# Performance work log

Hardware: AMD Instinct MI355X
Metric: run time of the kernel (lower is better)

Reference implementation:

```python
import jax, jax.numpy as jnp
import numpy as np

N_NODES = 50000
N_EDGES = 800000
IN_F = 128
HEADS = 8
D_HEAD = 16  # out_features // num_heads = 128 // 8


def setup_inputs() -> dict:
    key = jax.random.key(0)
    k1, k2, k3, k4, k5 = jax.random.split(key, 5)
    x = jax.random.normal(k1, (N_NODES, IN_F), dtype=jnp.float32)
    edge_index = jax.random.randint(k2, (2, N_EDGES), 0, N_NODES, dtype=jnp.int64)
    # nn.Linear weight is [out, in]; xavier-ish scale
    W = jax.random.normal(k3, (HEADS * D_HEAD, IN_F), dtype=jnp.float32) * (1.0 / np.sqrt(IN_F))
    a_src = jax.random.normal(k4, (HEADS, D_HEAD), dtype=jnp.float32) * (1.0 / np.sqrt(D_HEAD))
    a_dst = jax.random.normal(k5, (HEADS, D_HEAD), dtype=jnp.float32) * (1.0 / np.sqrt(D_HEAD))
    return {"x": x, "edge_index": edge_index, "W": W, "a_src": a_src, "a_dst": a_dst}


def reference(x, edge_index, W, a_src, a_dst):
    N = x.shape[0]
    H, D = a_src.shape
    # h = W x, reshaped to [N, H, D]
    h = (x @ W.T).reshape(N, H, D)
    src, dst = edge_index[0], edge_index[1]
    # per-node attention logits, then gather per-edge (same math as gathering h first)
    s_src = jnp.einsum("nhd,hd->nh", h, a_src)  # [N, H]
    s_dst = jnp.einsum("nhd,hd->nh", h, a_dst)  # [N, H]
    attn = jax.nn.leaky_relu(s_src[src] + s_dst[dst], negative_slope=0.2)  # [E, H]
    # torch scatter_reduce amax onto a zeros tensor -> max is clamped at 0
    attn_max = jnp.maximum(jax.ops.segment_max(attn, dst, num_segments=N), 0.0)  # [N, H]
    e = jnp.exp(attn - attn_max[dst])  # [E, H]
    attn_sum = jax.ops.segment_sum(e, dst, num_segments=N)  # [N, H]
    alpha = e / (attn_sum[dst] + 1e-10)  # [E, H] (dropout is identity in eval)
    msg = h[src] * alpha[..., None]  # [E, H, D]
    out = jax.ops.segment_sum(msg, dst, num_segments=N)  # [N, H, D]
    return out.reshape(N, H * D)
```

## Files before the change

kernel.cpp:

```cpp
#include <hip/hip_runtime.h>
#include <hip/hip_bf16.h>

#define N_NODES 50000
#define N_EDGES 800000
#define HEADS 8
#define MAXDEG 64
#define NPB 4
#define NMFMA ((N_NODES + 127) / 128)
#define NBINB 391
#define NBUCK 128
#define BUCK_NODES 391
#define BUCK_CAP 12288

using frag_ab = __attribute__((ext_vector_type(8))) short;
using frag_cd = __attribute__((ext_vector_type(4))) float;

static __device__ __forceinline__ short f2bs(float v) {
    __hip_bfloat16 b = __float2bfloat16(v);
    return *(short*)&b;
}

__global__ __launch_bounds__(256) void k_wc(const float* __restrict__ W,
                                            const float* __restrict__ a_src,
                                            const float* __restrict__ a_dst,
                                            __hip_bfloat16* __restrict__ Wcb,
                                            int* __restrict__ gcount) {
    int tid = blockIdx.x * 256 + threadIdx.x;
    if (tid < NBUCK) gcount[tid] = 0;
    if (tid >= 144 * 128) return;
    int r = tid >> 7, k = tid & 127;
    float v;
    if (r < 128) {
        v = W[tid];
    } else {
        int hd = (r - 128) & 7;
        const float* av = (r < 136) ? a_src : a_dst;
        v = 0.f;
        #pragma unroll
        for (int d = 0; d < 16; ++d)
            v += av[hd * 16 + d] * W[(size_t)(hd * 16 + d) * 128 + k];
    }
    Wcb[tid] = __float2bfloat16(v);
}

__global__ __launch_bounds__(256) void k_fm(const float* __restrict__ x,
                                            const __hip_bfloat16* __restrict__ Wcb,
                                            __hip_bfloat16* __restrict__ hb,
                                            float* __restrict__ s_src,
                                            float* __restrict__ s_dst,
                                            const int* __restrict__ ei,
                                            int* __restrict__ gcount,
                                            int2* __restrict__ bbuf) {
    __shared__ short Ws[144][136];
    const int t = threadIdx.x;

    if (blockIdx.x >= NMFMA) {
        __shared__ int hist[NBUCK];
        __shared__ int basei[NBUCK];
        const int fb = blockIdx.x - NMFMA;
        for (int i = t; i < NBUCK; i += 256) hist[i] = 0;
        __syncthreads();

        const int e0 = fb * 2048 + t * 8;
        const bool active = (e0 + 8 <= N_EDGES);
        int srcs[8], dsts[8], bks[8];
        if (active) {
            int4 s0 = *(const int4*)(ei + e0);
            int4 s1 = *(const int4*)(ei + e0 + 4);
            int4 d0 = *(const int4*)(ei + N_EDGES + e0);
            int4 d1 = *(const int4*)(ei + N_EDGES + e0 + 4);
            srcs[0] = s0.x; srcs[1] = s0.y; srcs[2] = s0.z; srcs[3] = s0.w;
            srcs[4] = s1.x; srcs[5] = s1.y; srcs[6] = s1.z; srcs[7] = s1.w;
            dsts[0] = d0.x; dsts[1] = d0.y; dsts[2] = d0.z; dsts[3] = d0.w;
            dsts[4] = d1.x; dsts[5] = d1.y; dsts[6] = d1.z; dsts[7] = d1.w;
            #pragma unroll
            for (int u = 0; u < 8; ++u) {
                bks[u] = dsts[u] / BUCK_NODES;
                atomicAdd(&hist[bks[u]], 1);
            }
        }
        __syncthreads();
        if (t < NBUCK) {
            int h = hist[t];
            basei[t] = h ? atomicAdd(&gcount[t], h) : 0;
            hist[t] = 0;
        }
        __syncthreads();
        if (active) {
            #pragma unroll
            for (int u = 0; u < 8; ++u) {
                int off = atomicAdd(&hist[bks[u]], 1);
                int pos = basei[bks[u]] + off;
                if (pos < BUCK_CAP)
                    bbuf[bks[u] * BUCK_CAP + pos] = make_int2(srcs[u], dsts[u]);
            }
        }
        return;
    }

    for (int i = t; i < 144 * 16; i += 256) {
        int r = i >> 4, c = (i & 15) << 3;
        frag_ab v = *(const frag_ab*)((const short*)Wcb + (size_t)r * 128 + c);
        *(frag_ab*)&Ws[r][c] = v;
    }
    __syncthreads();

    const int wave = t >> 6, lane = t & 63;
    const int rb0 = blockIdx.x * 128 + wave * 16;
    if (rb0 >= N_NODES) return;
    const int rb1 = rb0 + 64;
    const int m16 = lane & 15, kg = lane >> 4;
    const int arow0 = min(rb0 + m16, N_NODES - 1);
    const int arow1 = min(rb1 + m16, N_NODES - 1);
    const float* ab0 = x + (size_t)arow0 * 128 + kg * 8;
    const float* ab1 = x + (size_t)arow1 * 128 + kg * 8;

    frag_cd acc[2][9];
    #pragma unroll
    for (int r = 0; r < 2; ++r)
        #pragma unroll
        for (int j = 0; j < 9; ++j) acc[r][j] = (frag_cd){0.f, 0.f, 0.f, 0.f};

    #pragma unroll
    for (int ks = 0; ks < 4; ++ks) {
        float4 p0 = *(const float4*)(ab0 + ks * 32);
        float4 p1 = *(const float4*)(ab0 + ks * 32 + 4);
        float4 q0 = *(const float4*)(ab1 + ks * 32);
        float4 q1 = *(const float4*)(ab1 + ks * 32 + 4);
        frag_ab af0, af1;
        af0[0] = f2bs(p0.x); af0[1] = f2bs(p0.y); af0[2] = f2bs(p0.z); af0[3] = f2bs(p0.w);
        af0[4] = f2bs(p1.x); af0[5] = f2bs(p1.y); af0[6] = f2bs(p1.z); af0[7] = f2bs(p1.w);
        af1[0] = f2bs(q0.x); af1[1] = f2bs(q0.y); af1[2] = f2bs(q0.z); af1[3] = f2bs(q0.w);
        af1[4] = f2bs(q1.x); af1[5] = f2bs(q1.y); af1[6] = f2bs(q1.z); af1[7] = f2bs(q1.w);
        #pragma unroll
        for (int nt = 0; nt < 9; ++nt) {
            frag_ab bf = *(const frag_ab*)&Ws[nt * 16 + m16][ks * 32 + kg * 8];
            acc[0][nt] = __builtin_amdgcn_mfma_f32_16x16x32_bf16(af0, bf, acc[0][nt], 0, 0, 0);
            acc[1][nt] = __builtin_amdgcn_mfma_f32_16x16x32_bf16(af1, bf, acc[1][nt], 0, 0, 0);
        }
    }

    #pragma unroll
    for (int r = 0; r < 2; ++r) {
        int rbase = r ? rb1 : rb0;
        #pragma unroll
        for (int nt = 0; nt < 9; ++nt) {
            #pragma unroll
            for (int j = 0; j < 4; ++j) {
                int row = rbase + kg * 4 + j;
                if (row >= N_NODES) continue;
                int col = nt * 16 + m16;
                float v = acc[r][nt][j];
                if (col < 128)      hb[(size_t)row * 128 + col] = __float2bfloat16(v);
                else if (col < 136) s_src[row * 8 + (col - 128)] = v;
                else                s_dst[row * 8 + (col - 136)] = v;
            }
        }
    }
}

__global__ __launch_bounds__(256) void k_ell(const int2* __restrict__ bbuf,
                                             const int* __restrict__ gcount,
                                             int* __restrict__ cursor,
                                             int* __restrict__ csr_ell) {
    __shared__ int cur[BUCK_NODES];
    const int b = blockIdx.x;
    const int t = threadIdx.x;
    const int lo = b * BUCK_NODES;
    const int hi = min(lo + BUCK_NODES, N_NODES);
    const int ncur = hi - lo;
    for (int i = t; i < ncur; i += 256) cur[i] = 0;
    __syncthreads();
    const int cnt = min(gcount[b], BUCK_CAP);
    for (int i = t; i < cnt; i += 256) {
        int2 e = bbuf[(size_t)b * BUCK_CAP + i];
        int pos = atomicAdd(&cur[e.y - lo], 1);
        if (pos < MAXDEG) csr_ell[e.y * MAXDEG + pos] = e.x;
    }
    __syncthreads();
    for (int i = t; i < ncur; i += 256) cursor[lo + i] = cur[i];
}

__global__ __launch_bounds__(256) void k_gather(const int* __restrict__ csr_ell,
                                                const int* __restrict__ cursor,
                                                const float* __restrict__ s_src,
                                                const float* __restrict__ s_dst,
                                                const __hip_bfloat16* __restrict__ hb,
                                                float* __restrict__ out) {
    __shared__ int   csr_l[NPB][MAXDEG];
    __shared__ float sa[NPB][MAXDEG][9];
    const int slot = threadIdx.x >> 6;
    const int lane = threadIdx.x & 63;
    const int n = blockIdx.x * NPB + slot;
    if (n >= N_NODES) return;
    const int hd8 = lane >> 3, l8 = lane & 7;
    const int deg = min(cursor[n], MAXDEG);
    const float sdst = s_dst[n * 8 + hd8];

    if (lane < deg) csr_l[slot][lane] = csr_ell[n * MAXDEG + lane];

    float m = 0.f;
    for (int j = l8; j < deg; j += 8) {
        float a = s_src[csr_l[slot][j] * 8 + hd8] + sdst;
        a = a > 0.f ? a : 0.2f * a;
        sa[slot][j][hd8] = a;
        m = fmaxf(m, a);
    }
    #pragma unroll
    for (int mask = 1; mask <= 4; mask <<= 1)
        m = fmaxf(m, __shfl_xor(m, mask));

    float s = 0.f;
    for (int j = l8; j < deg; j += 8) {
        float w = __expf(sa[slot][j][hd8] - m);
        sa[slot][j][hd8] = w;
        s += w;
    }
    #pragma unroll
    for (int mask = 1; mask <= 4; mask <<= 1)
        s += __shfl_xor(s, mask);
    float rcp = 1.0f / (s + 1e-10f);

    const int q = lane >> 4;
    const int fl = lane & 15;
    const int hd = fl >> 1;
    const float rcpq = __shfl(rcp, hd * 8);

    const unsigned short* hbs = (const unsigned short*)hb;
    float acc[8] = {0.f, 0.f, 0.f, 0.f, 0.f, 0.f, 0.f, 0.f};

    int j = 0;
    for (; j + 16 <= deg; j += 16) {
        int  jj0 = j + q,      jj1 = j + 4 + q,  jj2 = j + 8 + q,  jj3 = j + 12 + q;
        int  s0 = csr_l[slot][jj0], s1 = csr_l[slot][jj1];
        int  s2 = csr_l[slot][jj2], s3 = csr_l[slot][jj3];
        float w0 = sa[slot][jj0][hd], w1 = sa[slot][jj1][hd];
        float w2 = sa[slot][jj2][hd], w3 = sa[slot][jj3][hd];
        uint4 v0 = *(const uint4*)(hbs + (size_t)s0 * 128 + fl * 8);
        uint4 v1 = *(const uint4*)(hbs + (size_t)s1 * 128 + fl * 8);
        uint4 v2 = *(const uint4*)(hbs + (size_t)s2 * 128 + fl * 8);
        uint4 v3 = *(const uint4*)(hbs + (size_t)s3 * 128 + fl * 8);
        #define ACC8(vv, ww) \
            acc[0] += (ww) * __uint_as_float((vv).x << 16); \
            acc[1] += (ww) * __uint_as_float((vv).x & 0xffff0000u); \
            acc[2] += (ww) * __uint_as_float((vv).y << 16); \
            acc[3] += (ww) * __uint_as_float((vv).y & 0xffff0000u); \
            acc[4] += (ww) * __uint_as_float((vv).z << 16); \
            acc[5] += (ww) * __uint_as_float((vv).z & 0xffff0000u); \
            acc[6] += (ww) * __uint_as_float((vv).w << 16); \
            acc[7] += (ww) * __uint_as_float((vv).w & 0xffff0000u);
        ACC8(v0, w0) ACC8(v1, w1) ACC8(v2, w2) ACC8(v3, w3)
    }
    for (; j + 4 <= deg; j += 4) {
        int jj = j + q;
        int src = csr_l[slot][jj];
        float w = sa[slot][jj][hd];
        uint4 v = *(const uint4*)(hbs + (size_t)src * 128 + fl * 8);
        ACC8(v, w)
    }
    if (j < deg) {
        int jj = j + q;
        if (jj < deg) {
            int src = csr_l[slot][jj];
            float w = sa[slot][jj][hd];
            uint4 v = *(const uint4*)(hbs + (size_t)src * 128 + fl * 8);
            ACC8(v, w)
        }
    }
    #undef ACC8

    #pragma unroll
    for (int k = 0; k < 8; ++k) {
        acc[k] += __shfl_xor(acc[k], 16);
        acc[k] += __shfl_xor(acc[k], 32);
    }
    if (q == 0) {
        float4 o0 = { acc[0] * rcpq, acc[1] * rcpq, acc[2] * rcpq, acc[3] * rcpq };
        float4 o1 = { acc[4] * rcpq, acc[5] * rcpq, acc[6] * rcpq, acc[7] * rcpq };
        *(float4*)(out + (size_t)n * 128 + fl * 8)     = o0;
        *(float4*)(out + (size_t)n * 128 + fl * 8 + 4) = o1;
    }
}

extern "C" void kernel_launch(void* const* d_in, const int* in_sizes, int n_in,
                              void* d_out, int out_size, void* d_ws, size_t ws_size,
                              hipStream_t stream) {
    const float* x     = (const float*)d_in[0];
    const int*   ei    = (const int*)d_in[1];
    const float* W     = (const float*)d_in[2];
    const float* a_src = (const float*)d_in[3];
    const float* a_dst = (const float*)d_in[4];
    float* out = (float*)d_out;

    char* ws = (char*)d_ws;
    __hip_bfloat16* hb      = (__hip_bfloat16*)(ws);
    __hip_bfloat16* Wcb     = (__hip_bfloat16*)(ws + 12800000);
    float*          s_src   = (float*)(ws + 12840000);
    float*          s_dst   = (float*)(ws + 14440000);
    int*            cursor  = (int*)  (ws + 16040000);
    int*            gcount  = (int*)  (ws + 16240000);
    int*            csr_ell = (int*)  (ws + 16241024);
    int2*           bbuf    = (int2*) (ws + 29041024);

    k_wc    <<<(144 * 128 + 255) / 256, 256, 0, stream>>>(W, a_src, a_dst, Wcb, gcount);
    k_fm    <<<NMFMA + NBINB, 256, 0, stream>>>(x, Wcb, hb, s_src, s_dst, ei, gcount, bbuf);
    k_ell   <<<NBUCK, 256, 0, stream>>>(bbuf, gcount, cursor, csr_ell);
    k_gather<<<(N_NODES + NPB - 1) / NPB, 256, 0, stream>>>(csr_ell, cursor, s_src, s_dst, hb, out);
}
```

Baseline: 84.15 us.

## Fold weight prep into GEMM kernel, drop softmax max pass, pad gather loop

Removes the separate weight-combination kernel. Each GEMM block now converts W to bf16 and computes the a_src/a_dst projected rows directly into shared memory, and the bucket counters are cleared with a memset. In the gather kernel, the softmax max-subtraction pass is dropped so exponentials are taken directly on the logits. The edge loop is also padded to multiples of 16 with zero weights, which removes the remainder loops. The trade-offs are redundant per-block weight computation and a risk of exp overflow if logits become large.

```diff
diff --git a/kernel.cpp b/kernel.cpp
--- a/kernel.cpp
+++ b/kernel.cpp
@@ -20,31 +20,10 @@
     return *(short*)&b;
 }
 
-__global__ __launch_bounds__(256) void k_wc(const float* __restrict__ W,
+__global__ __launch_bounds__(256) void k_fm(const float* __restrict__ x,
+                                            const float* __restrict__ W,
                                             const float* __restrict__ a_src,
                                             const float* __restrict__ a_dst,
-                                            __hip_bfloat16* __restrict__ Wcb,
-                                            int* __restrict__ gcount) {
-    int tid = blockIdx.x * 256 + threadIdx.x;
-    if (tid < NBUCK) gcount[tid] = 0;
-    if (tid >= 144 * 128) return;
-    int r = tid >> 7, k = tid & 127;
-    float v;
-    if (r < 128) {
-        v = W[tid];
-    } else {
-        int hd = (r - 128) & 7;
-        const float* av = (r < 136) ? a_src : a_dst;
-        v = 0.f;
-        #pragma unroll
-        for (int d = 0; d < 16; ++d)
-            v += av[hd * 16 + d] * W[(size_t)(hd * 16 + d) * 128 + k];
-    }
-    Wcb[tid] = __float2bfloat16(v);
-}
-
-__global__ __launch_bounds__(256) void k_fm(const float* __restrict__ x,
-                                            const __hip_bfloat16* __restrict__ Wcb,
                                             __hip_bfloat16* __restrict__ hb,
                                             float* __restrict__ s_src,
                                             float* __restrict__ s_dst,
@@ -98,10 +77,24 @@
         return;
     }
 
-    for (int i = t; i < 144 * 16; i += 256) {
+    for (int i = t; i < 128 * 16; i += 256) {
         int r = i >> 4, c = (i & 15) << 3;
-        frag_ab v = *(const frag_ab*)((const short*)Wcb + (size_t)r * 128 + c);
+        float4 w0 = *(const float4*)(W + r * 128 + c);
+        float4 w1 = *(const float4*)(W + r * 128 + c + 4);
+        frag_ab v;
+        v[0] = f2bs(w0.x); v[1] = f2bs(w0.y); v[2] = f2bs(w0.z); v[3] = f2bs(w0.w);
+        v[4] = f2bs(w1.x); v[5] = f2bs(w1.y); v[6] = f2bs(w1.z); v[7] = f2bs(w1.w);
         *(frag_ab*)&Ws[r][c] = v;
+    }
+    for (int i = t; i < 16 * 128; i += 256) {
+        int rr = i >> 7, k = i & 127;
+        int hd = rr & 7;
+        const float* av = (rr < 8) ? a_src : a_dst;
+        float v = 0.f;
+        #pragma unroll
+        for (int d = 0; d < 16; ++d)
+            v += av[hd * 16 + d] * W[(size_t)(hd * 16 + d) * 128 + k];
+        Ws[128 + rr][k] = f2bs(v);
     }
     __syncthreads();
 
@@ -195,27 +188,21 @@
     if (n >= N_NODES) return;
     const int hd8 = lane >> 3, l8 = lane & 7;
     const int deg = min(cursor[n], MAXDEG);
+    const int degPad = (deg + 15) & ~15;
     const float sdst = s_dst[n * 8 + hd8];
 
-    if (lane < deg) csr_l[slot][lane] = csr_ell[n * MAXDEG + lane];
-
-    float m = 0.f;
+    if (lane < degPad) csr_l[slot][lane] = (lane < deg) ? csr_ell[n * MAXDEG + lane] : 0;
+
+    float s = 0.f;
     for (int j = l8; j < deg; j += 8) {
         float a = s_src[csr_l[slot][j] * 8 + hd8] + sdst;
         a = a > 0.f ? a : 0.2f * a;
-        sa[slot][j][hd8] = a;
-        m = fmaxf(m, a);
-    }
-    #pragma unroll
-    for (int mask = 1; mask <= 4; mask <<= 1)
-        m = fmaxf(m, __shfl_xor(m, mask));
-
-    float s = 0.f;
-    for (int j = l8; j < deg; j += 8) {
-        float w = __expf(sa[slot][j][hd8] - m);
+        float w = __expf(a);
         sa[slot][j][hd8] = w;
         s += w;
     }
+    for (int j = deg + hd8; j < degPad; j += 8)
+        sa[slot][j][l8] = 0.f;
     #pragma unroll
     for (int mask = 1; mask <= 4; mask <<= 1)
         s += __shfl_xor(s, mask);
@@ -229,8 +216,9 @@
     const unsigned short* hbs = (const unsigned short*)hb;
     float acc[8] = {0.f, 0.f, 0.f, 0.f, 0.f, 0.f, 0.f, 0.f};
 
-    int j = 0;
-    for (; j + 16 <= deg; j += 16) {
+    const int nIter = degPad >> 4;
+    for (int it = 0; it < nIter; ++it) {
+        const int j = it << 4;
         int  jj0 = j + q,      jj1 = j + 4 + q,  jj2 = j + 8 + q,  jj3 = j + 12 + q;
         int  s0 = csr_l[slot][jj0], s1 = csr_l[slot][jj1];
         int  s2 = csr_l[slot][jj2], s3 = csr_l[slot][jj3];
@@ -250,24 +238,8 @@
             acc[6] += (ww) * __uint_as_float((vv).w << 16); \
             acc[7] += (ww) * __uint_as_float((vv).w & 0xffff0000u);
         ACC8(v0, w0) ACC8(v1, w1) ACC8(v2, w2) ACC8(v3, w3)
-    }
-    for (; j + 4 <= deg; j += 4) {
-        int jj = j + q;
-        int src = csr_l[slot][jj];
-        float w = sa[slot][jj][hd];
-        uint4 v = *(const uint4*)(hbs + (size_t)src * 128 + fl * 8);
-        ACC8(v, w)
-    }
-    if (j < deg) {
-        int jj = j + q;
-        if (jj < deg) {
-            int src = csr_l[slot][jj];
-            float w = sa[slot][jj][hd];
-            uint4 v = *(const uint4*)(hbs + (size_t)src * 128 + fl * 8);
-            ACC8(v, w)
-        }
-    }
-    #undef ACC8
+        #undef ACC8
+    }
 
     #pragma unroll
     for (int k = 0; k < 8; ++k) {
@@ -294,16 +266,15 @@
 
     char* ws = (char*)d_ws;
     __hip_bfloat16* hb      = (__hip_bfloat16*)(ws);
-    __hip_bfloat16* Wcb     = (__hip_bfloat16*)(ws + 12800000);
-    float*          s_src   = (float*)(ws + 12840000);
-    float*          s_dst   = (float*)(ws + 14440000);
-    int*            cursor  = (int*)  (ws + 16040000);
-    int*            gcount  = (int*)  (ws + 16240000);
-    int*            csr_ell = (int*)  (ws + 16241024);
-    int2*           bbuf    = (int2*) (ws + 29041024);
-
-    k_wc    <<<(144 * 128 + 255) / 256, 256, 0, stream>>>(W, a_src, a_dst, Wcb, gcount);
-    k_fm    <<<NMFMA + NBINB, 256, 0, stream>>>(x, Wcb, hb, s_src, s_dst, ei, gcount, bbuf);
+    float*          s_src   = (float*)(ws + 12800000);
+    float*          s_dst   = (float*)(ws + 14400000);
+    int*            cursor  = (int*)  (ws + 16000000);
+    int*            gcount  = (int*)  (ws + 16200000);
+    int*            csr_ell = (int*)  (ws + 16200512);
+    int2*           bbuf    = (int2*) (ws + 29000512);
+
+    hipMemsetAsync(gcount, 0, NBUCK * 4, stream);
+    k_fm    <<<NMFMA + NBINB, 256, 0, stream>>>(x, W, a_src, a_dst, hb, s_src, s_dst, ei, gcount, bbuf);
     k_ell   <<<NBUCK, 256, 0, stream>>>(bbuf, gcount, cursor, csr_ell);
     k_gather<<<(N_NODES + NPB - 1) / NPB, 256, 0, stream>>>(csr_ell, cursor, s_src, s_dst, hb, out);
 }
```

Result: no change. 85.32 us (+1.4%).
